# Kernel optimization log

Measured on AMD Instinct MI355X. Metric: run time of the kernel, lower is better.

## Reference

```python
import jax, jax.numpy as jnp
import numpy as np
import math

BATCH, SEQ, HIDDEN, HEADS = 2, 2048, 1024, 16
HEAD_SIZE = HIDDEN // HEADS
NEG_INF = -10000.0  # faithful to the torch module's masking constant


def setup_inputs() -> dict:
    key = jax.random.key(0)
    k1, k2, k3, k4 = jax.random.split(key, 4)
    x = jax.random.normal(k1, (BATCH, SEQ, HIDDEN), dtype=jnp.float32)
    pos_table = jax.random.normal(k2, (SEQ, HIDDEN), dtype=jnp.float32) * 0.02
    # torch nn.Linear weight layout: [out_features, in_features]
    Wqkv = jax.random.normal(k3, (3 * HIDDEN, HIDDEN), dtype=jnp.float32) * (1.0 / math.sqrt(HIDDEN))
    Wout = jax.random.normal(k4, (HIDDEN, HIDDEN), dtype=jnp.float32) * (1.0 / math.sqrt(HIDDEN))
    return {"x": x, "pos_table": pos_table, "Wqkv": Wqkv, "Wout": Wout}


def reference(x, pos_table, Wqkv, Wout):
    b, n, h = x.shape
    # positional embedding added for Q/K projection only (V uses raw x)
    xp = x + pos_table[None, :n, :]
    qk = jnp.einsum('bnd,ed->bne', xp, Wqkv[: 2 * HIDDEN])          # [b, n, 2h]
    q, k = jnp.split(qk, 2, axis=-1)
    v = jnp.einsum('bnd,ed->bne', x, Wqkv[2 * HIDDEN:])             # [b, n, h]

    def to_heads(t):  # b n (h l) -> b h n l
        return t.reshape(b, n, HEADS, HEAD_SIZE).transpose(0, 2, 1, 3)

    q, k, v = to_heads(q), to_heads(k), to_heads(v)

    scores = jnp.einsum('bhql,bhkl->bhqk', q, k) / math.sqrt(HEAD_SIZE)
    q_ind = jnp.arange(n)[:, None]
    k_ind = jnp.arange(n)[None, :]
    mask = q_ind < k_ind                                            # True where future
    scores = jnp.where(mask, NEG_INF, scores)
    probs = jax.nn.softmax(scores, axis=-1)
    combined_v = jnp.einsum('bhqk,bhkl->bhql', probs, v)            # [b, h, n, l]
    combined_v = combined_v.transpose(0, 2, 1, 3).reshape(b, n, h)  # b h q l -> b q (h l)
    out = jnp.einsum('bnd,ed->bne', combined_v, Wout)
    return out
```

## Files before the change

### kernel.cpp

```cpp
#include <hip/hip_runtime.h>
#include <hip/hip_bf16.h>
#include <stdint.h>

#define BATCH 2
#define SEQ   2048
#define HID   1024
#define NHEAD 16
#define HD    64
#define MROWS (BATCH*SEQ)

typedef __attribute__((ext_vector_type(8))) short bf16x8;
typedef __attribute__((ext_vector_type(4))) float f32x4;

__device__ inline unsigned short f2bf(float f){
  union { float f; unsigned u; } v; v.f = f;
  unsigned r = v.u + 0x7fffu + ((v.u >> 16) & 1u);
  return (unsigned short)(r >> 16);
}
__device__ inline unsigned packbf(float a, float b){
  return (unsigned)f2bf(a) | ((unsigned)f2bf(b) << 16);
}
__device__ inline void lds_load16(const short* g, short* l){
  __builtin_amdgcn_global_load_lds(
      (const __attribute__((address_space(1))) void*)g,
      (__attribute__((address_space(3))) void*)l, 16, 0, 0);
}

__global__ __launch_bounds__(256) void cast_xpos(
    const float* __restrict__ x, const float* __restrict__ pos,
    short* __restrict__ xb, short* __restrict__ xv){
  int i = blockIdx.x * 256 + threadIdx.x;
  float4 xa = ((const float4*)x)[i];
  float4 pa = ((const float4*)pos)[i & (SEQ*HID/4 - 1)];
  short4 sb, sv;
  sb.x = (short)f2bf(xa.x + pa.x); sb.y = (short)f2bf(xa.y + pa.y);
  sb.z = (short)f2bf(xa.z + pa.z); sb.w = (short)f2bf(xa.w + pa.w);
  sv.x = (short)f2bf(xa.x); sv.y = (short)f2bf(xa.y);
  sv.z = (short)f2bf(xa.z); sv.w = (short)f2bf(xa.w);
  ((short4*)xb)[i] = sb;
  ((short4*)xv)[i] = sv;
}

__global__ __launch_bounds__(256) void cast_wmat(
    const float* __restrict__ in, short* __restrict__ out){
  int i = blockIdx.x * 256 + threadIdx.x;
  float4 a = ((const float4*)in)[i];
  short4 s;
  s.x = (short)f2bf(a.x); s.y = (short)f2bf(a.y);
  s.z = (short)f2bf(a.z); s.w = (short)f2bf(a.w);
  ((short4*)out)[i] = s;
}

template<bool F32OUT>
__global__ __launch_bounds__(256) void gemm_bt(
    const short* __restrict__ A0, const short* __restrict__ A1, int split_bx,
    const short* __restrict__ W, void* __restrict__ Cout, int K, int ldc,
    int qsb, float qscale){
  __shared__ alignas(16) short As[2][128*32];
  __shared__ alignas(16) short Bs[2][128*32];
  const int bx = blockIdx.x, by = blockIdx.y;
  const short* A = (bx < split_bx) ? A0 : A1;
  const int tid  = threadIdx.x;
  const int w    = tid >> 6, lane = tid & 63;
  const int g    = lane >> 4, c = lane & 15;
  const int wr   = w >> 1, wc = w & 1;

  f32x4 acc[4][4];
#pragma unroll
  for (int m = 0; m < 4; ++m)
#pragma unroll
    for (int n = 0; n < 4; ++n) acc[m][n] = (f32x4){0.f, 0.f, 0.f, 0.f};

  const short* Abase = A + (size_t)(by*128) * K;
  const short* Wbase = W + (size_t)(bx*128) * K;

  auto stage = [&](int buf, int kt){
#pragma unroll
    for (int j = 0; j < 2; ++j){
      int ci  = w*128 + j*64 + lane;
      int row = ci >> 2, sub = ci & 3;
      lds_load16(Abase + (size_t)row*K + kt + sub*8, &As[buf][(w*128 + j*64)*8]);
      lds_load16(Wbase + (size_t)row*K + kt + sub*8, &Bs[buf][(w*128 + j*64)*8]);
    }
  };

  const int nk = K >> 5;
  stage(0, 0);
  int buf = 0;
  for (int ki = 0; ki < nk; ++ki){
    __syncthreads();
    if (ki + 1 < nk) stage(buf ^ 1, (ki + 1) * 32);

    bf16x8 af[4], bfr[4];
#pragma unroll
    for (int m = 0; m < 4; ++m)
      af[m] = *(const bf16x8*)&As[buf][(wr*64 + m*16 + c)*32 + g*8];
#pragma unroll
    for (int n = 0; n < 4; ++n)
      bfr[n] = *(const bf16x8*)&Bs[buf][(wc*64 + n*16 + c)*32 + g*8];
    __builtin_amdgcn_s_setprio(1);
#pragma unroll
    for (int m = 0; m < 4; ++m)
#pragma unroll
      for (int n = 0; n < 4; ++n)
        acc[m][n] = __builtin_amdgcn_mfma_f32_16x16x32_bf16(af[m], bfr[n], acc[m][n], 0, 0, 0);
    __builtin_amdgcn_s_setprio(0);
    buf ^= 1;
  }

  const float sc = (bx < qsb) ? qscale : 1.0f;
  const int row0 = by*128 + wr*64;
  const int col0 = bx*128 + wc*64;
#pragma unroll
  for (int m = 0; m < 4; ++m)
#pragma unroll
    for (int n = 0; n < 4; ++n)
#pragma unroll
      for (int r = 0; r < 4; ++r){
        size_t idx = (size_t)(row0 + m*16 + g*4 + r) * ldc + (col0 + n*16 + c);
        if constexpr (F32OUT) ((float*)Cout)[idx] = acc[m][n][r] * sc;
        else                  ((short*)Cout)[idx] = (short)f2bf(acc[m][n][r] * sc);
      }
}

__global__ __launch_bounds__(256) void attn_fwd(
    const short* __restrict__ qkv, short* __restrict__ out){
  const int bid = blockIdx.x;
  const int qt  = 31 - (bid >> 5);
  const int bh  = bid & 31;
  const int b   = bh >> 4, h = bh & 15;
  const int tid = threadIdx.x;
  const int w   = tid >> 6, lane = tid & 63;
  const int g   = lane >> 4, c = lane & 15;

  __shared__ alignas(16) short Ks[2][64*64];
  __shared__ alignas(16) short Vt[2][64*64];

  const int q0 = qt*64 + w*16;
  const size_t rowb = (size_t)b * SEQ;

  const short* qptr = qkv + (rowb + q0 + c)*3072 + h*HD;
  bf16x8 qf0 = *(const bf16x8*)(qptr + g*8);
  bf16x8 qf1 = *(const bf16x8*)(qptr + 32 + g*8);

  const short* kbase = qkv + rowb*3072 + HID   + h*HD;
  const short* vbase = qkv + rowb*3072 + 2*HID + h*HD;

  const int slot   = ((lane >> 5) << 5) | (((lane >> 2) & 3) << 3)
                   | (((lane >> 4) & 1) << 2) | (lane & 3);
  const int vchunk = slot >> 3, vcol = slot & 7;

  auto stageK = [&](int buf, int c0){
#pragma unroll
    for (int j = 0; j < 2; ++j){
      int pc  = w*128 + j*64 + lane;
      int row = pc >> 3;
      int lc  = (pc & 7) ^ (row & 7);
      lds_load16(kbase + (size_t)(c0 + row)*3072 + lc*8, &Ks[buf][(w*128 + j*64)*8]);
    }
  };
  auto loadV = [&](int c0, bf16x8& v0, bf16x8& v1){
    const short* vp = vbase + (size_t)(c0 + lane)*3072 + w*16;
    v0 = *(const bf16x8*)(vp);
    v1 = *(const bf16x8*)(vp + 8);
  };
  auto scatterV = [&](int buf, const bf16x8& v0, const bf16x8& v1){
#pragma unroll
    for (int j = 0; j < 8; ++j)
      Vt[buf][(w*16 + j)*64 + ((vchunk ^ (j & 7)) << 3) + vcol] = v0[j];
#pragma unroll
    for (int j = 0; j < 8; ++j)
      Vt[buf][(w*16 + 8 + j)*64 + ((vchunk ^ ((8 + j) & 7)) << 3) + vcol] = v1[j];
  };

  f32x4 ot[4];
#pragma unroll
  for (int dt = 0; dt < 4; ++dt) ot[dt] = (f32x4){0.f, 0.f, 0.f, 0.f};
  float mrow = -1e30f, lrow = 0.f;
  const int qg = q0 + c;

  {
    bf16x8 v0, v1;
    stageK(0, 0);
    loadV(0, v0, v1);
    scatterV(0, v0, v1);
  }
  int cur = 0;
  for (int ch = 0; ch <= qt; ++ch){
    const int c0 = ch * 64;
    __syncthreads();

    bf16x8 nv0, nv1;
    if (ch < qt){
      stageK(cur ^ 1, c0 + 64);
      loadV(c0 + 64, nv0, nv1);
    }

    f32x4 s[4];
    __builtin_amdgcn_s_setprio(1);
#pragma unroll
    for (int kt = 0; kt < 4; ++kt){
      int row = kt*16 + c;
      bf16x8 k0 = *(const bf16x8*)&Ks[cur][row*64 + ((g       ^ (row&7))<<3)];
      bf16x8 k1 = *(const bf16x8*)&Ks[cur][row*64 + (((4 + g) ^ (row&7))<<3)];
      f32x4 z = (f32x4){0.f, 0.f, 0.f, 0.f};
      s[kt] = __builtin_amdgcn_mfma_f32_16x16x32_bf16(k0, qf0, z, 0, 0, 0);
      s[kt] = __builtin_amdgcn_mfma_f32_16x16x32_bf16(k1, qf1, s[kt], 0, 0, 0);
    }
    __builtin_amdgcn_s_setprio(0);

    float pv[16];
#pragma unroll
    for (int kt = 0; kt < 4; ++kt)
#pragma unroll
      for (int r = 0; r < 4; ++r) pv[kt*4 + r] = s[kt][r];

    if (ch == qt){
#pragma unroll
      for (int kt = 0; kt < 4; ++kt)
#pragma unroll
        for (int r = 0; r < 4; ++r){
          int ki = c0 + kt*16 + g*4 + r;
          if (ki > qg) pv[kt*4 + r] = -1e30f;
        }
    }

    float cm = fmaxf(fmaxf(fmaxf(pv[0], pv[1]), fmaxf(pv[2], pv[3])),
                     fmaxf(fmaxf(pv[4], pv[5]), fmaxf(pv[6], pv[7])));
    cm = fmaxf(cm, fmaxf(fmaxf(fmaxf(pv[8], pv[9]), fmaxf(pv[10], pv[11])),
                         fmaxf(fmaxf(pv[12], pv[13]), fmaxf(pv[14], pv[15]))));
    cm = fmaxf(cm, __shfl_xor(cm, 16));
    cm = fmaxf(cm, __shfl_xor(cm, 32));
    if (__any(cm > mrow + 5.5f)){
      float mnew  = fmaxf(mrow, cm);
      float alpha = __expf(mrow - mnew);
      lrow *= alpha;
#pragma unroll
      for (int dt = 0; dt < 4; ++dt)
#pragma unroll
        for (int r = 0; r < 4; ++r) ot[dt][r] *= alpha;
      mrow = mnew;
    }
    float ps = 0.f;
#pragma unroll
    for (int i = 0; i < 16; ++i){ pv[i] = __expf(pv[i] - mrow); ps += pv[i]; }
    ps += __shfl_xor(ps, 16);
    ps += __shfl_xor(ps, 32);
    lrow += ps;

    union { unsigned u[4]; bf16x8 v; } pb0, pb1;
    pb0.u[0] = packbf(pv[0],  pv[1]);  pb0.u[1] = packbf(pv[2],  pv[3]);
    pb0.u[2] = packbf(pv[4],  pv[5]);  pb0.u[3] = packbf(pv[6],  pv[7]);
    pb1.u[0] = packbf(pv[8],  pv[9]);  pb1.u[1] = packbf(pv[10], pv[11]);
    pb1.u[2] = packbf(pv[12], pv[13]); pb1.u[3] = packbf(pv[14], pv[15]);

    __builtin_amdgcn_s_setprio(1);
#pragma unroll
    for (int dt = 0; dt < 4; ++dt){
      int d = dt*16 + c;
      bf16x8 va0 = *(const bf16x8*)&Vt[cur][d*64 + ((g       ^ (d&7))<<3)];
      bf16x8 va1 = *(const bf16x8*)&Vt[cur][d*64 + (((4 + g) ^ (d&7))<<3)];
      ot[dt] = __builtin_amdgcn_mfma_f32_16x16x32_bf16(va0, pb0.v, ot[dt], 0, 0, 0);
      ot[dt] = __builtin_amdgcn_mfma_f32_16x16x32_bf16(va1, pb1.v, ot[dt], 0, 0, 0);
    }
    __builtin_amdgcn_s_setprio(0);

    if (ch < qt) scatterV(cur ^ 1, nv0, nv1);
    cur ^= 1;
  }

  float inv = 1.f / lrow;
  short* obase = out + (rowb + q0 + c)*HID + h*HD + g*4;
#pragma unroll
  for (int dt = 0; dt < 4; ++dt){
    uint2 uu;
    uu.x = packbf(ot[dt][0]*inv, ot[dt][1]*inv);
    uu.y = packbf(ot[dt][2]*inv, ot[dt][3]*inv);
    *(uint2*)(obase + dt*16) = uu;
  }
}

extern "C" void kernel_launch(void* const* d_in, const int* in_sizes, int n_in,
                              void* d_out, int out_size, void* d_ws, size_t ws_size,
                              hipStream_t stream){
  const float* x    = (const float*)d_in[0];
  const float* pos  = (const float*)d_in[1];
  const float* Wqkv = (const float*)d_in[2];
  const float* Wout = (const float*)d_in[3];

  short* xb     = (short*)d_ws;
  short* xv     = xb    + (size_t)MROWS*HID;
  short* wqkvb  = xv    + (size_t)MROWS*HID;
  short* woutb  = wqkvb + (size_t)3*HID*HID;
  short* qkv    = woutb + (size_t)HID*HID;
  short* attn_o = xb;

  cast_xpos<<<dim3(MROWS*HID/1024), 256, 0, stream>>>(x, pos, xb, xv);
  cast_wmat<<<dim3(3*HID*HID/1024), 256, 0, stream>>>(Wqkv, wqkvb);
  cast_wmat<<<dim3(HID*HID/1024),   256, 0, stream>>>(Wout, woutb);

  gemm_bt<false><<<dim3(24, 32), 256, 0, stream>>>(xb, xv, 16, wqkvb, qkv, HID, 3*HID,
                                                   8, 0.125f);

  attn_fwd<<<dim3(1024), 256, 0, stream>>>(qkv, attn_o);

  gemm_bt<true><<<dim3(8, 32), 256, 0, stream>>>(attn_o, attn_o, 8, woutb, d_out, HID, HID,
                                                 0, 1.0f);
}
```

Baseline: 201.5 us.

## Fold log2e into Q scale, use exp2, packed bf16 casts, merge weight casts

Folds log2(e) into the Q scaling factor so the softmax can use the native exp2 instruction in place of __expf, and raises the lazy-rescale threshold to match the base-2 domain. Replaces the manual bf16 rounding with the packed two-wide conversion intrinsic across the cast, GEMM-epilogue and attention kernels. Merges the two weight-cast launches into one kernel. The max reduction is also regrouped into three-input maxes. Together these are meant to cut VALU work and one launch, at the cost of small numeric differences.

Result: faster. 197.1 us (-2.2%).

```diff
diff --git a/kernel.cpp b/kernel.cpp
--- a/kernel.cpp
+++ b/kernel.cpp
@@ -12,13 +12,17 @@
 typedef __attribute__((ext_vector_type(8))) short bf16x8;
 typedef __attribute__((ext_vector_type(4))) float f32x4;
 
-__device__ inline unsigned short f2bf(float f){
-  union { float f; unsigned u; } v; v.f = f;
-  unsigned r = v.u + 0x7fffu + ((v.u >> 16) & 1u);
-  return (unsigned short)(r >> 16);
-}
-__device__ inline unsigned packbf(float a, float b){
-  return (unsigned)f2bf(a) | ((unsigned)f2bf(b) << 16);
+__device__ inline unsigned pk2(float a, float b){
+  __hip_bfloat162 h = __float22bfloat162_rn(make_float2(a, b));
+  union { __hip_bfloat162 h; unsigned u; } v; v.h = h;
+  return v.u;
+}
+__device__ inline float fexp2(float x){
+#if __has_builtin(__builtin_amdgcn_exp2f)
+  return __builtin_amdgcn_exp2f(x);
+#else
+  return exp2f(x);
+#endif
 }
 __device__ inline void lds_load16(const short* g, short* l){
   __builtin_amdgcn_global_load_lds(
@@ -32,23 +36,28 @@
   int i = blockIdx.x * 256 + threadIdx.x;
   float4 xa = ((const float4*)x)[i];
   float4 pa = ((const float4*)pos)[i & (SEQ*HID/4 - 1)];
-  short4 sb, sv;
-  sb.x = (short)f2bf(xa.x + pa.x); sb.y = (short)f2bf(xa.y + pa.y);
-  sb.z = (short)f2bf(xa.z + pa.z); sb.w = (short)f2bf(xa.w + pa.w);
-  sv.x = (short)f2bf(xa.x); sv.y = (short)f2bf(xa.y);
-  sv.z = (short)f2bf(xa.z); sv.w = (short)f2bf(xa.w);
-  ((short4*)xb)[i] = sb;
-  ((short4*)xv)[i] = sv;
-}
-
-__global__ __launch_bounds__(256) void cast_wmat(
-    const float* __restrict__ in, short* __restrict__ out){
+  uint2 sb, sv;
+  sb.x = pk2(xa.x + pa.x, xa.y + pa.y);
+  sb.y = pk2(xa.z + pa.z, xa.w + pa.w);
+  sv.x = pk2(xa.x, xa.y);
+  sv.y = pk2(xa.z, xa.w);
+  ((uint2*)xb)[i] = sb;
+  ((uint2*)xv)[i] = sv;
+}
+
+__global__ __launch_bounds__(256) void cast_w2(
+    const float* __restrict__ w1, const float* __restrict__ w2,
+    short* __restrict__ o1, short* __restrict__ o2){
   int i = blockIdx.x * 256 + threadIdx.x;
-  float4 a = ((const float4*)in)[i];
-  short4 s;
-  s.x = (short)f2bf(a.x); s.y = (short)f2bf(a.y);
-  s.z = (short)f2bf(a.z); s.w = (short)f2bf(a.w);
-  ((short4*)out)[i] = s;
+  const int n1 = 3*HID*HID/4;
+  const float4* src; uint2* dst; int j;
+  if (i < n1){ src = (const float4*)w1; dst = (uint2*)o1; j = i; }
+  else       { src = (const float4*)w2; dst = (uint2*)o2; j = i - n1; }
+  float4 a = src[j];
+  uint2 s;
+  s.x = pk2(a.x, a.y);
+  s.y = pk2(a.z, a.w);
+  dst[j] = s;
 }
 
 template<bool F32OUT>
@@ -114,13 +123,22 @@
 #pragma unroll
   for (int m = 0; m < 4; ++m)
 #pragma unroll
-    for (int n = 0; n < 4; ++n)
-#pragma unroll
-      for (int r = 0; r < 4; ++r){
-        size_t idx = (size_t)(row0 + m*16 + g*4 + r) * ldc + (col0 + n*16 + c);
-        if constexpr (F32OUT) ((float*)Cout)[idx] = acc[m][n][r] * sc;
-        else                  ((short*)Cout)[idx] = (short)f2bf(acc[m][n][r] * sc);
+    for (int n = 0; n < 4; ++n){
+      size_t base = (size_t)(row0 + m*16 + g*4) * ldc + (col0 + n*16 + c);
+      if constexpr (F32OUT){
+#pragma unroll
+        for (int r = 0; r < 4; ++r)
+          ((float*)Cout)[base + (size_t)r*ldc] = acc[m][n][r] * sc;
+      } else {
+        short* p = (short*)Cout + base;
+        unsigned u01 = pk2(acc[m][n][0]*sc, acc[m][n][1]*sc);
+        unsigned u23 = pk2(acc[m][n][2]*sc, acc[m][n][3]*sc);
+        p[0]             = (short)(u01 & 0xffff);
+        p[(size_t)ldc]   = (short)(u01 >> 16);
+        p[2*(size_t)ldc] = (short)(u23 & 0xffff);
+        p[3*(size_t)ldc] = (short)(u23 >> 16);
       }
+    }
 }
 
 __global__ __launch_bounds__(256) void attn_fwd(
@@ -225,15 +243,17 @@
         }
     }
 
-    float cm = fmaxf(fmaxf(fmaxf(pv[0], pv[1]), fmaxf(pv[2], pv[3])),
-                     fmaxf(fmaxf(pv[4], pv[5]), fmaxf(pv[6], pv[7])));
-    cm = fmaxf(cm, fmaxf(fmaxf(fmaxf(pv[8], pv[9]), fmaxf(pv[10], pv[11])),
-                         fmaxf(fmaxf(pv[12], pv[13]), fmaxf(pv[14], pv[15]))));
+    float a0 = fmaxf(fmaxf(pv[0],  pv[1]),  pv[2]);
+    float a1 = fmaxf(fmaxf(pv[3],  pv[4]),  pv[5]);
+    float a2 = fmaxf(fmaxf(pv[6],  pv[7]),  pv[8]);
+    float a3 = fmaxf(fmaxf(pv[9],  pv[10]), pv[11]);
+    float a4 = fmaxf(fmaxf(pv[12], pv[13]), pv[14]);
+    float cm = fmaxf(fmaxf(fmaxf(a0, a1), a2), fmaxf(fmaxf(a3, a4), pv[15]));
     cm = fmaxf(cm, __shfl_xor(cm, 16));
     cm = fmaxf(cm, __shfl_xor(cm, 32));
-    if (__any(cm > mrow + 5.5f)){
+    if (__any(cm > mrow + 8.0f)){
       float mnew  = fmaxf(mrow, cm);
-      float alpha = __expf(mrow - mnew);
+      float alpha = fexp2(mrow - mnew);
       lrow *= alpha;
 #pragma unroll
       for (int dt = 0; dt < 4; ++dt)
@@ -243,16 +263,16 @@
     }
     float ps = 0.f;
 #pragma unroll
-    for (int i = 0; i < 16; ++i){ pv[i] = __expf(pv[i] - mrow); ps += pv[i]; }
+    for (int i = 0; i < 16; ++i){ pv[i] = fexp2(pv[i] - mrow); ps += pv[i]; }
     ps += __shfl_xor(ps, 16);
     ps += __shfl_xor(ps, 32);
     lrow += ps;
 
     union { unsigned u[4]; bf16x8 v; } pb0, pb1;
-    pb0.u[0] = packbf(pv[0],  pv[1]);  pb0.u[1] = packbf(pv[2],  pv[3]);
-    pb0.u[2] = packbf(pv[4],  pv[5]);  pb0.u[3] = packbf(pv[6],  pv[7]);
-    pb1.u[0] = packbf(pv[8],  pv[9]);  pb1.u[1] = packbf(pv[10], pv[11]);
-    pb1.u[2] = packbf(pv[12], pv[13]); pb1.u[3] = packbf(pv[14], pv[15]);
+    pb0.u[0] = pk2(pv[0],  pv[1]);  pb0.u[1] = pk2(pv[2],  pv[3]);
+    pb0.u[2] = pk2(pv[4],  pv[5]);  pb0.u[3] = pk2(pv[6],  pv[7]);
+    pb1.u[0] = pk2(pv[8],  pv[9]);  pb1.u[1] = pk2(pv[10], pv[11]);
+    pb1.u[2] = pk2(pv[12], pv[13]); pb1.u[3] = pk2(pv[14], pv[15]);
 
     __builtin_amdgcn_s_setprio(1);
 #pragma unroll
@@ -274,8 +294,8 @@
 #pragma unroll
   for (int dt = 0; dt < 4; ++dt){
     uint2 uu;
-    uu.x = packbf(ot[dt][0]*inv, ot[dt][1]*inv);
-    uu.y = packbf(ot[dt][2]*inv, ot[dt][3]*inv);
+    uu.x = pk2(ot[dt][0]*inv, ot[dt][1]*inv);
+    uu.y = pk2(ot[dt][2]*inv, ot[dt][3]*inv);
     *(uint2*)(obase + dt*16) = uu;
   }
 }
@@ -296,11 +316,10 @@
   short* attn_o = xb;
 
   cast_xpos<<<dim3(MROWS*HID/1024), 256, 0, stream>>>(x, pos, xb, xv);
-  cast_wmat<<<dim3(3*HID*HID/1024), 256, 0, stream>>>(Wqkv, wqkvb);
-  cast_wmat<<<dim3(HID*HID/1024),   256, 0, stream>>>(Wout, woutb);
+  cast_w2<<<dim3(4*HID*HID/1024), 256, 0, stream>>>(Wqkv, Wout, wqkvb, woutb);
 
   gemm_bt<false><<<dim3(24, 32), 256, 0, stream>>>(xb, xv, 16, wqkvb, qkv, HID, 3*HID,
-                                                   8, 0.125f);
+                                                   8, 0.18033688011112042f);
 
   attn_fwd<<<dim3(1024), 256, 0, stream>>>(qkv, attn_o);
 
```
